# Kernel optimization log

Hardware: AMD Instinct MI355X
Metric: run time of the kernel (lower is better)

The kernel has to match this reference:

```python
import jax, jax.numpy as jnp
import numpy as np

HIDDEN = 1024
HEADS = 16
HEAD_DIM = HIDDEN // HEADS
SCALE = HEAD_DIM ** -0.5
NEG_INF = -1e9  # finite stand-in for -inf so silu(masked) -> ~0 instead of NaN


def setup_inputs() -> dict:
    key = jax.random.key(0)
    ks = jax.random.split(key, 12)
    B, Sq, Sk = 2, 2048, 2048
    inp = {
        "query": jax.random.normal(ks[0], (B, Sq, HIDDEN), jnp.float32),
        "key": jax.random.normal(ks[1], (B, Sk, HIDDEN), jnp.float32),
        "value": jax.random.normal(ks[2], (B, Sk, HIDDEN), jnp.float32),
        "mask": jax.random.randint(ks[3], (B, 1, Sq, Sk), 0, 2, jnp.int32),
        # torch nn.Linear weights are [out_features, in_features]
        "Wq": jax.random.normal(ks[4], (HIDDEN, HIDDEN), jnp.float32) * 0.02,
        "bq": jax.random.normal(ks[5], (HIDDEN,), jnp.float32) * 0.02,
        "Wk": jax.random.normal(ks[6], (HIDDEN, HIDDEN), jnp.float32) * 0.02,
        "bk": jax.random.normal(ks[7], (HIDDEN,), jnp.float32) * 0.02,
        "Wv": jax.random.normal(ks[8], (HIDDEN, HIDDEN), jnp.float32) * 0.02,
        "bv": jax.random.normal(ks[9], (HIDDEN,), jnp.float32) * 0.02,
        "Wo": jax.random.normal(ks[10], (HIDDEN, HIDDEN), jnp.float32) * 0.02,
    }
    return inp


def _split_heads(x):
    B, S, _ = x.shape
    return x.reshape(B, S, HEADS, HEAD_DIM).transpose(0, 2, 1, 3)  # [B,H,S,D]


def reference(query, key, value, mask, Wq, bq, Wk, bk, Wv, bv, Wo):
    B, Sq, _ = query.shape
    q = _split_heads(query @ Wq.T + bq)   # [B,H,Sq,D]
    k = _split_heads(key @ Wk.T + bk)     # [B,H,Sk,D]
    v = _split_heads(value @ Wv.T + bv)   # [B,H,Sk,D]
    scores = jnp.einsum("bhqd,bhkd->bhqk", q, k) * SCALE
    scores = jnp.where(mask == 0, NEG_INF, scores)
    attn = jax.nn.silu(scores)            # silu in place of softmax (per source)
    # dropout is identity in eval mode
    out = jnp.einsum("bhqk,bhkd->bhqd", attn, v)
    out = out.transpose(0, 2, 1, 3).reshape(B, Sq, HIDDEN)
    return out @ Wo.T  # o_proj has no bias
```

## Files before the change

kernel.cpp:

```cpp
#include <hip/hip_runtime.h>
#include <hip/hip_bf16.h>

typedef __attribute__((ext_vector_type(4))) float f32x4;
typedef __attribute__((ext_vector_type(16))) float f32x16;
typedef __attribute__((ext_vector_type(8))) short short8;
typedef __attribute__((ext_vector_type(4))) unsigned int uint4v;

__device__ __forceinline__ unsigned short f2bf(float f) {
  unsigned int u = __float_as_uint(f);
  u += 0x7fffu + ((u >> 16) & 1u);
  return (unsigned short)(u >> 16);
}

__device__ __forceinline__ void g2lds16(const void* g, void* l) {
  __builtin_amdgcn_global_load_lds(
      (const __attribute__((address_space(1))) void*)g,
      (__attribute__((address_space(3))) void*)l, 16, 0, 0);
}

__global__ __launch_bounds__(256) void cvt3(const float* __restrict__ s0,
                                            const float* __restrict__ s1,
                                            const float* __restrict__ s2,
                                            unsigned short* __restrict__ d0,
                                            unsigned short* __restrict__ d1,
                                            unsigned short* __restrict__ d2) {
  const int i = blockIdx.x * 256 + threadIdx.x;
  const float* s = blockIdx.y == 0 ? s0 : (blockIdx.y == 1 ? s1 : s2);
  unsigned short* d = blockIdx.y == 0 ? d0 : (blockIdx.y == 1 ? d1 : d2);
  const float4 v = ((const float4*)s)[i];
  ushort4 o;
  o.x = f2bf(v.x); o.y = f2bf(v.y); o.z = f2bf(v.z); o.w = f2bf(v.w);
  ((ushort4*)d)[i] = o;
}

__global__ __launch_bounds__(256) void cvt4(const float* __restrict__ s0,
                                            const float* __restrict__ s1,
                                            const float* __restrict__ s2,
                                            const float* __restrict__ s3,
                                            unsigned short* __restrict__ d0,
                                            unsigned short* __restrict__ d1,
                                            unsigned short* __restrict__ d2,
                                            unsigned short* __restrict__ d3) {
  const int i = blockIdx.x * 256 + threadIdx.x;
  const float* s = blockIdx.y == 0 ? s0 : (blockIdx.y == 1 ? s1 : (blockIdx.y == 2 ? s2 : s3));
  unsigned short* d = blockIdx.y == 0 ? d0 : (blockIdx.y == 1 ? d1 : (blockIdx.y == 2 ? d2 : d3));
  const float4 v = ((const float4*)s)[i];
  ushort4 o;
  o.x = f2bf(v.x); o.y = f2bf(v.y); o.z = f2bf(v.z); o.w = f2bf(v.w);
  ((ushort4*)d)[i] = o;
}

__global__ __launch_bounds__(256) void pack_mask(const int* __restrict__ mask,
                                                 unsigned long long* __restrict__ mb) {
  int i = blockIdx.x * 256 + threadIdx.x;
  unsigned long long bits = __ballot(mask[i] != 0);
  if ((threadIdx.x & 63) == 0) mb[i >> 6] = bits;
}

__global__ __launch_bounds__(256) void add_bf16(const unsigned short* __restrict__ a,
                                                const unsigned short* __restrict__ b,
                                                unsigned short* __restrict__ o) {
  const int i = blockIdx.x * 256 + threadIdx.x;
  const short8 va = ((const short8*)a)[i];
  const short8 vb = ((const short8*)b)[i];
  short8 vo;
#pragma unroll
  for (int j = 0; j < 8; ++j) {
    const float fa = __uint_as_float((unsigned int)(unsigned short)va[j] << 16);
    const float fb = __uint_as_float((unsigned int)(unsigned short)vb[j] << 16);
    vo[j] = (short)f2bf(fa + fb);
  }
  ((short8*)o)[i] = vo;
}

template <int BIAS_MODE, int OUT_BF16>
__device__ __forceinline__ void gemm_tile(
    unsigned short* __restrict__ As, unsigned short* __restrict__ Bs,
    const unsigned short* __restrict__ A, const unsigned short* __restrict__ B,
    const float* __restrict__ bias, void* __restrict__ Cp,
    const int N, const int K, const int m0, const int n0, const float cscale) {
  const int tid  = (int)threadIdx.x;
  const int lane = tid & 63;
  const int wm   = tid >> 7;
  const int wn   = (tid >> 6) & 1;

  const f32x4 vzero = {0.f, 0.f, 0.f, 0.f};
  f32x4 acc[4][4];
#pragma unroll
  for (int mr = 0; mr < 4; ++mr)
#pragma unroll
    for (int nr = 0; nr < 4; ++nr) acc[mr][nr] = vzero;

  for (int k0 = 0; k0 < K; k0 += 64) {
#pragma unroll
    for (int i = 0; i < 4; ++i) {
      const int idx = i * 256 + tid;
      const int r = idx >> 3;
      const int c = idx & 7;
      const int koff = k0 + ((c ^ (r & 7)) << 3);
      g2lds16(A + (size_t)(m0 + r) * K + koff, &As[(i * 256 + (tid & 192)) * 8]);
      g2lds16(B + (size_t)(n0 + r) * K + koff, &Bs[(i * 256 + (tid & 192)) * 8]);
    }
    __syncthreads();
#pragma unroll
    for (int kk = 0; kk < 2; ++kk) {
      short8 af[4], bf[4];
#pragma unroll
      for (int mr = 0; mr < 4; ++mr) {
        const int row = wm * 64 + mr * 16 + (lane & 15);
        const int ch = (kk * 4 + (lane >> 4)) ^ (row & 7);
        af[mr] = *(const short8*)&As[row * 64 + ch * 8];
      }
#pragma unroll
      for (int nr = 0; nr < 4; ++nr) {
        const int row = wn * 64 + nr * 16 + (lane & 15);
        const int ch = (kk * 4 + (lane >> 4)) ^ (row & 7);
        bf[nr] = *(const short8*)&Bs[row * 64 + ch * 8];
      }
#pragma unroll
      for (int mr = 0; mr < 4; ++mr)
#pragma unroll
        for (int nr = 0; nr < 4; ++nr)
          acc[mr][nr] = __builtin_amdgcn_mfma_f32_16x16x32_bf16(af[mr], bf[nr],
                                                                acc[mr][nr], 0, 0, 0);
    }
    __syncthreads();
  }

#pragma unroll
  for (int mr = 0; mr < 4; ++mr) {
#pragma unroll
    for (int nr = 0; nr < 4; ++nr) {
#pragma unroll
      for (int rg = 0; rg < 4; ++rg) {
        const int row = m0 + wm * 64 + mr * 16 + ((lane >> 4) << 2) + rg;
        const int col = n0 + wn * 64 + nr * 16 + (lane & 15);
        float v = acc[mr][nr][rg];
        if (BIAS_MODE == 1) v += bias[col];
        if (BIAS_MODE == 2) v += bias[row];
        v *= cscale;
        if (OUT_BF16) ((unsigned short*)Cp)[(size_t)row * N + col] = f2bf(v);
        else          ((float*)Cp)[(size_t)row * N + col] = v;
      }
    }
  }
}

#define QSCALE 0.18033688011112042f
#define LN2    0.6931471805599453f

__global__ __launch_bounds__(256) void proj_qkv(
    const unsigned short* __restrict__ xq, const unsigned short* __restrict__ xk,
    const unsigned short* __restrict__ xv,
    const unsigned short* __restrict__ wq, const unsigned short* __restrict__ wk,
    const unsigned short* __restrict__ wv,
    const float* __restrict__ bq, const float* __restrict__ bk,
    const float* __restrict__ bv,
    unsigned short* __restrict__ qp, unsigned short* __restrict__ kp,
    unsigned short* __restrict__ vt) {
  __shared__ unsigned short As[128 * 64];
  __shared__ unsigned short Bs[128 * 64];
  const int z = blockIdx.z;
  if (z == 0) {
    gemm_tile<1, 1>(As, Bs, xq, wq, bq, qp, 1024, 1024, blockIdx.y * 128, blockIdx.x * 128, QSCALE);
  } else if (z == 1) {
    gemm_tile<1, 1>(As, Bs, xk, wk, bk, kp, 1024, 1024, blockIdx.y * 128, blockIdx.x * 128, 1.0f);
  } else {
    gemm_tile<2, 1>(As, Bs, wv, xv, bv, vt, 4096, 1024, blockIdx.x * 128, blockIdx.y * 128, 1.0f);
  }
}

__global__ __launch_bounds__(256) void out_proj(
    const unsigned short* __restrict__ ao, const unsigned short* __restrict__ wo,
    float* __restrict__ out) {
  __shared__ unsigned short As[128 * 64];
  __shared__ unsigned short Bs[128 * 64];
  gemm_tile<0, 0>(As, Bs, ao, wo, nullptr, out, 1024, 1024, blockIdx.y * 128, blockIdx.x * 128, 1.0f);
}

__global__ __launch_bounds__(256, 4) void attn_kernel(
    const unsigned short* __restrict__ qp, const unsigned short* __restrict__ kp,
    const unsigned short* __restrict__ vt, const unsigned long long* __restrict__ mb,
    unsigned short* __restrict__ ao0, unsigned short* __restrict__ ao1) {
  __shared__ unsigned short Ks[2][64 * 64];
  __shared__ unsigned short Vts[2][64 * 64];

  const int tid  = (int)threadIdx.x;
  const int lane = tid & 63;
  const int w    = tid >> 6;
  const int c32  = lane & 31;
  const int lo   = lane >> 5;
  const int qbase = blockIdx.x * 128;
  const int h  = blockIdx.y;
  const int b  = blockIdx.z >> 1;
  const int ks = blockIdx.z & 1;
  const size_t tok0 = (size_t)b * 2048;
  const int kbase = ks * 1024;

  const int q = qbase + w * 32 + c32;
  const unsigned short* qptr = qp + (tok0 + q) * 1024 + h * 64 + lo * 8;
  short8 qf[4];
#pragma unroll
  for (int kd = 0; kd < 4; ++kd) qf[kd] = *(const short8*)(qptr + kd * 16);

  const unsigned long long* mql = mb + (tok0 + q) * 32 + ks * 16;

  f32x16 oacc[2];
#pragma unroll
  for (int dt = 0; dt < 2; ++dt)
#pragma unroll
    for (int r = 0; r < 16; ++r) oacc[dt][r] = 0.f;

  auto stage = [&](int kt_, int bf_) {
#pragma unroll
    for (int i = 0; i < 2; ++i) {
      const int idx = i * 256 + tid;
      const int r = idx >> 3;
      const int cc = idx & 7;
      const int cs = (cc ^ (r & 7)) << 3;
      g2lds16(kp + (tok0 + kbase + kt_ * 64 + r) * 1024 + h * 64 + cs,
              &Ks[bf_][(i * 256 + (tid & 192)) * 8]);
      g2lds16(vt + (size_t)(h * 64 + r) * 4096 + tok0 + kbase + kt_ * 64 + cs,
              &Vts[bf_][(i * 256 + (tid & 192)) * 8]);
    }
  };

  stage(0, 0);
  unsigned long long mcur = mql[0];
  __syncthreads();

  const f32x16 z16 = {0.f};
  int buf = 0;
  for (int kt = 0; kt < 16; ++kt) {
    if (kt < 15) stage(kt + 1, buf ^ 1);
    const unsigned long long mnext = (kt < 15) ? mql[kt + 1] : 0ULL;

    f32x16 st[2];
    st[0] = z16; st[1] = z16;
    __builtin_amdgcn_s_setprio(1);
#pragma unroll
    for (int kd = 0; kd < 4; ++kd) {
      const int ch = ((2 * kd + lo) ^ (c32 & 7)) << 3;
      const short8 kf0 = *(const short8*)&Ks[buf][c32 * 64 + ch];
      const short8 kf1 = *(const short8*)&Ks[buf][(32 + c32) * 64 + ch];
      st[0] = __builtin_amdgcn_mfma_f32_32x32x16_bf16(kf0, qf[kd], st[0], 0, 0, 0);
      st[1] = __builtin_amdgcn_mfma_f32_32x32x16_bf16(kf1, qf[kd], st[1], 0, 0, 0);
    }
    __builtin_amdgcn_s_setprio(0);

#pragma unroll
    for (int t = 0; t < 2; ++t) {
      const unsigned int ms = (unsigned int)(mcur >> (t * 32 + lo * 4));
#pragma unroll
      for (int r = 0; r < 16; ++r) {
        const int krow = (r & 3) + 8 * (r >> 2);
        const int smear = __builtin_amdgcn_sbfe((int)ms, krow, 1);
        const float sv = __int_as_float(__float_as_int(st[t][r]) & smear);
        st[t][r] = sv * __builtin_amdgcn_rcpf(1.f + __builtin_amdgcn_exp2f(-sv));
      }

      unsigned int u[8];
#pragma unroll
      for (int g = 0; g < 4; ++g) {
        asm("v_cvt_pk_bf16_f32 %0, %1, %2" : "=v"(u[2 * g])     : "v"(st[t][4 * g]),     "v"(st[t][4 * g + 1]));
        asm("v_cvt_pk_bf16_f32 %0, %1, %2" : "=v"(u[2 * g + 1]) : "v"(st[t][4 * g + 2]), "v"(st[t][4 * g + 3]));
      }
      asm("v_permlane32_swap_b32 %0, %1" : "+v"(u[0]), "+v"(u[2]));
      asm("v_permlane32_swap_b32 %0, %1" : "+v"(u[1]), "+v"(u[3]));
      asm("v_permlane32_swap_b32 %0, %1" : "+v"(u[4]), "+v"(u[6]));
      asm("v_permlane32_swap_b32 %0, %1" : "+v"(u[5]), "+v"(u[7]));
      const uint4v wA = {u[0], u[1], u[2], u[3]};
      const uint4v wB = {u[4], u[5], u[6], u[7]};
      const short8 paA = __builtin_bit_cast(short8, wA);
      const short8 paB = __builtin_bit_cast(short8, wB);

      __builtin_amdgcn_s_setprio(1);
#pragma unroll
      for (int dt = 0; dt < 2; ++dt) {
        const int drow = dt * 32 + c32;
        const short8 vf0 = *(const short8*)&Vts[buf][drow * 64 + (((4 * t + lo) ^ (c32 & 7)) << 3)];
        const short8 vf1 = *(const short8*)&Vts[buf][drow * 64 + (((4 * t + 2 + lo) ^ (c32 & 7)) << 3)];
        oacc[dt] = __builtin_amdgcn_mfma_f32_32x32x16_bf16(paA, vf0, oacc[dt], 0, 0, 0);
        oacc[dt] = __builtin_amdgcn_mfma_f32_32x32x16_bf16(paB, vf1, oacc[dt], 0, 0, 0);
      }
      __builtin_amdgcn_s_setprio(0);
    }

    mcur = mnext;
    __syncthreads();
    buf ^= 1;
  }

  unsigned short* aop = ks ? ao1 : ao0;
#pragma unroll
  for (int dt = 0; dt < 2; ++dt) {
#pragma unroll
    for (int r = 0; r < 16; ++r) {
      const int row = qbase + w * 32 + (r & 3) + 8 * (r >> 2) + 4 * lo;
      const int col = h * 64 + dt * 32 + c32;
      aop[(tok0 + row) * 1024 + col] = f2bf(oacc[dt][r] * LN2);
    }
  }
}

extern "C" void kernel_launch(void* const* d_in, const int* in_sizes, int n_in,
                              void* d_out, int out_size, void* d_ws, size_t ws_size,
                              hipStream_t stream) {
  (void)in_sizes; (void)n_in; (void)out_size; (void)ws_size;
  const float* query = (const float*)d_in[0];
  const float* key   = (const float*)d_in[1];
  const float* value = (const float*)d_in[2];
  const int*   mask  = (const int*)d_in[3];
  const float* Wq = (const float*)d_in[4];
  const float* bq = (const float*)d_in[5];
  const float* Wk = (const float*)d_in[6];
  const float* bk = (const float*)d_in[7];
  const float* Wv = (const float*)d_in[8];
  const float* bv = (const float*)d_in[9];
  const float* Wo = (const float*)d_in[10];

  char* ws = (char*)d_ws;
  const size_t MB = 1024 * 1024;
  unsigned short* xq  = (unsigned short*)(ws + 0 * MB);
  unsigned short* xk  = (unsigned short*)(ws + 8 * MB);
  unsigned short* xv  = (unsigned short*)(ws + 16 * MB);
  unsigned short* wqb = (unsigned short*)(ws + 24 * MB);
  unsigned short* wkb = (unsigned short*)(ws + 26 * MB);
  unsigned short* wvb = (unsigned short*)(ws + 28 * MB);
  unsigned short* wob = (unsigned short*)(ws + 30 * MB);
  unsigned short* qp  = (unsigned short*)(ws + 32 * MB);
  unsigned short* kp  = (unsigned short*)(ws + 40 * MB);
  unsigned short* vt  = (unsigned short*)(ws + 48 * MB);
  unsigned long long* mbq = (unsigned long long*)(ws + 56 * MB);
  unsigned short* ao  = xq;
  unsigned short* ap0 = xk;
  unsigned short* ap1 = xv;

  cvt3<<<dim3(4096, 3), 256, 0, stream>>>(query, key, value, xq, xk, xv);
  cvt4<<<dim3(1024, 4), 256, 0, stream>>>(Wq, Wk, Wv, Wo, wqb, wkb, wvb, wob);
  pack_mask<<<32768, 256, 0, stream>>>(mask, mbq);

  proj_qkv<<<dim3(8, 32, 3), 256, 0, stream>>>(xq, xk, xv, wqb, wkb, wvb,
                                               bq, bk, bv, qp, kp, vt);
  attn_kernel<<<dim3(16, 16, 4), 256, 0, stream>>>(qp, kp, vt, mbq, ap0, ap1);
  add_bf16<<<2048, 256, 0, stream>>>(ap0, ap1, ao);
  out_proj<<<dim3(8, 32), 256, 0, stream>>>(ao, wob, (float*)d_out);
}
```

Before: 171.5 us.

## Split key dimension across extra waves in attention and out-projection, fuse prep kernels

```diff
diff --git a/kernel.cpp b/kernel.cpp
--- a/kernel.cpp
+++ b/kernel.cpp
@@ -18,43 +18,42 @@
       (__attribute__((address_space(3))) void*)l, 16, 0, 0);
 }
 
-__global__ __launch_bounds__(256) void cvt3(const float* __restrict__ s0,
-                                            const float* __restrict__ s1,
-                                            const float* __restrict__ s2,
-                                            unsigned short* __restrict__ d0,
-                                            unsigned short* __restrict__ d1,
-                                            unsigned short* __restrict__ d2) {
-  const int i = blockIdx.x * 256 + threadIdx.x;
-  const float* s = blockIdx.y == 0 ? s0 : (blockIdx.y == 1 ? s1 : s2);
-  unsigned short* d = blockIdx.y == 0 ? d0 : (blockIdx.y == 1 ? d1 : d2);
-  const float4 v = ((const float4*)s)[i];
+__global__ __launch_bounds__(256) void prep(
+    const float* __restrict__ q, const float* __restrict__ k,
+    const float* __restrict__ v, const float* __restrict__ Wq,
+    const float* __restrict__ Wk, const float* __restrict__ Wv,
+    const float* __restrict__ Wo, const int* __restrict__ mask,
+    unsigned short* __restrict__ xq, unsigned short* __restrict__ xk,
+    unsigned short* __restrict__ xv, unsigned short* __restrict__ wqb,
+    unsigned short* __restrict__ wkb, unsigned short* __restrict__ wvb,
+    unsigned short* __restrict__ wob, unsigned long long* __restrict__ mb) {
+  const int y = blockIdx.y;
+  const int idx = blockIdx.x * 256 + (int)threadIdx.x;
+  if (y == 4) {
+#pragma unroll
+    for (int it = 0; it < 8; ++it) {
+      const int i = blockIdx.x * 2048 + it * 256 + (int)threadIdx.x;
+      const unsigned long long bits = __ballot(mask[i] != 0);
+      if ((threadIdx.x & 63) == 0) mb[i >> 6] = bits;
+    }
+    return;
+  }
+  const float* s;
+  unsigned short* d;
+  int i = idx;
+  if (y == 0)      { s = q; d = xq; }
+  else if (y == 1) { s = k; d = xk; }
+  else if (y == 2) { s = v; d = xv; }
+  else {
+    const int wsel = idx >> 18;
+    i = idx & 0x3FFFF;
+    s = wsel == 0 ? Wq : (wsel == 1 ? Wk : (wsel == 2 ? Wv : Wo));
+    d = wsel == 0 ? wqb : (wsel == 1 ? wkb : (wsel == 2 ? wvb : wob));
+  }
+  const float4 val = ((const float4*)s)[i];
   ushort4 o;
-  o.x = f2bf(v.x); o.y = f2bf(v.y); o.z = f2bf(v.z); o.w = f2bf(v.w);
+  o.x = f2bf(val.x); o.y = f2bf(val.y); o.z = f2bf(val.z); o.w = f2bf(val.w);
   ((ushort4*)d)[i] = o;
-}
-
-__global__ __launch_bounds__(256) void cvt4(const float* __restrict__ s0,
-                                            const float* __restrict__ s1,
-                                            const float* __restrict__ s2,
-                                            const float* __restrict__ s3,
-                                            unsigned short* __restrict__ d0,
-                                            unsigned short* __restrict__ d1,
-                                            unsigned short* __restrict__ d2,
-                                            unsigned short* __restrict__ d3) {
-  const int i = blockIdx.x * 256 + threadIdx.x;
-  const float* s = blockIdx.y == 0 ? s0 : (blockIdx.y == 1 ? s1 : (blockIdx.y == 2 ? s2 : s3));
-  unsigned short* d = blockIdx.y == 0 ? d0 : (blockIdx.y == 1 ? d1 : (blockIdx.y == 2 ? d2 : d3));
-  const float4 v = ((const float4*)s)[i];
-  ushort4 o;
-  o.x = f2bf(v.x); o.y = f2bf(v.y); o.z = f2bf(v.z); o.w = f2bf(v.w);
-  ((ushort4*)d)[i] = o;
-}
-
-__global__ __launch_bounds__(256) void pack_mask(const int* __restrict__ mask,
-                                                 unsigned long long* __restrict__ mb) {
-  int i = blockIdx.x * 256 + threadIdx.x;
-  unsigned long long bits = __ballot(mask[i] != 0);
-  if ((threadIdx.x & 63) == 0) mb[i >> 6] = bits;
 }
 
 __global__ __launch_bounds__(256) void add_bf16(const unsigned short* __restrict__ a,
@@ -170,24 +169,104 @@
   }
 }
 
-__global__ __launch_bounds__(256) void out_proj(
+__global__ __launch_bounds__(512) void out_proj8(
     const unsigned short* __restrict__ ao, const unsigned short* __restrict__ wo,
     float* __restrict__ out) {
-  __shared__ unsigned short As[128 * 64];
-  __shared__ unsigned short Bs[128 * 64];
-  gemm_tile<0, 0>(As, Bs, ao, wo, nullptr, out, 1024, 1024, blockIdx.y * 128, blockIdx.x * 128, 1.0f);
-}
-
-__global__ __launch_bounds__(256, 4) void attn_kernel(
+  __shared__ unsigned short SM[4][128 * 64];
+
+  const int tid  = (int)threadIdx.x;
+  const int lane = tid & 63;
+  const int wm = tid >> 8;
+  const int wn = (tid >> 7) & 1;
+  const int kh = (tid >> 6) & 1;
+  const int m0 = blockIdx.y * 128;
+  const int n0 = blockIdx.x * 128;
+
+  const f32x4 vzero = {0.f, 0.f, 0.f, 0.f};
+  f32x4 acc[4][4];
+#pragma unroll
+  for (int mr = 0; mr < 4; ++mr)
+#pragma unroll
+    for (int nr = 0; nr < 4; ++nr) acc[mr][nr] = vzero;
+
+  for (int j = 0; j < 8; ++j) {
+#pragma unroll
+    for (int i = 0; i < 2; ++i) {
+      const int idx = i * 512 + tid;
+      const int r = idx >> 3;
+      const int cc = idx & 7;
+      const int cs = (cc ^ (r & 7)) << 3;
+      const int wb = (i * 512 + (tid & 448)) * 8;
+      g2lds16(ao + (size_t)(m0 + r) * 1024 + j * 64 + cs,       &SM[0][wb]);
+      g2lds16(ao + (size_t)(m0 + r) * 1024 + 512 + j * 64 + cs, &SM[1][wb]);
+      g2lds16(wo + (size_t)(n0 + r) * 1024 + j * 64 + cs,       &SM[2][wb]);
+      g2lds16(wo + (size_t)(n0 + r) * 1024 + 512 + j * 64 + cs, &SM[3][wb]);
+    }
+    __syncthreads();
+#pragma unroll
+    for (int kk = 0; kk < 2; ++kk) {
+      short8 af[4], bf[4];
+#pragma unroll
+      for (int mr = 0; mr < 4; ++mr) {
+        const int row = wm * 64 + mr * 16 + (lane & 15);
+        const int ch = (kk * 4 + (lane >> 4)) ^ (row & 7);
+        af[mr] = *(const short8*)&SM[kh][row * 64 + ch * 8];
+      }
+#pragma unroll
+      for (int nr = 0; nr < 4; ++nr) {
+        const int row = wn * 64 + nr * 16 + (lane & 15);
+        const int ch = (kk * 4 + (lane >> 4)) ^ (row & 7);
+        bf[nr] = *(const short8*)&SM[2 + kh][row * 64 + ch * 8];
+      }
+#pragma unroll
+      for (int mr = 0; mr < 4; ++mr)
+#pragma unroll
+        for (int nr = 0; nr < 4; ++nr)
+          acc[mr][nr] = __builtin_amdgcn_mfma_f32_16x16x32_bf16(af[mr], bf[nr],
+                                                                acc[mr][nr], 0, 0, 0);
+    }
+    __syncthreads();
+  }
+
+  float* red = (float*)SM;
+  const int reg4 = wm * 2 + wn;
+  if (kh) {
+#pragma unroll
+    for (int mr = 0; mr < 4; ++mr)
+#pragma unroll
+      for (int nr = 0; nr < 4; ++nr)
+#pragma unroll
+        for (int g = 0; g < 4; ++g)
+          red[reg4 * 4096 + lane * 64 + ((mr * 16 + nr * 4 + g + lane) & 63)] = acc[mr][nr][g];
+  }
+  __syncthreads();
+  if (!kh) {
+#pragma unroll
+    for (int mr = 0; mr < 4; ++mr)
+#pragma unroll
+      for (int nr = 0; nr < 4; ++nr)
+#pragma unroll
+        for (int g = 0; g < 4; ++g) {
+          const float v = acc[mr][nr][g] +
+              red[reg4 * 4096 + lane * 64 + ((mr * 16 + nr * 4 + g + lane) & 63)];
+          const int row = m0 + wm * 64 + mr * 16 + ((lane >> 4) << 2) + g;
+          const int col = n0 + wn * 64 + nr * 16 + (lane & 15);
+          out[(size_t)row * 1024 + col] = v;
+        }
+  }
+}
+
+__global__ __launch_bounds__(512, 4) void attn_kernel(
     const unsigned short* __restrict__ qp, const unsigned short* __restrict__ kp,
     const unsigned short* __restrict__ vt, const unsigned long long* __restrict__ mb,
     unsigned short* __restrict__ ao0, unsigned short* __restrict__ ao1) {
-  __shared__ unsigned short Ks[2][64 * 64];
-  __shared__ unsigned short Vts[2][64 * 64];
+  __shared__ unsigned short SMEM[2][2][64 * 64];
 
   const int tid  = (int)threadIdx.x;
   const int lane = tid & 63;
   const int w    = tid >> 6;
+  const int qsub = w >> 1;
+  const int kh   = w & 1;
   const int c32  = lane & 31;
   const int lo   = lane >> 5;
   const int qbase = blockIdx.x * 128;
@@ -197,7 +276,7 @@
   const size_t tok0 = (size_t)b * 2048;
   const int kbase = ks * 1024;
 
-  const int q = qbase + w * 32 + c32;
+  const int q = qbase + qsub * 32 + c32;
   const unsigned short* qptr = qp + (tok0 + q) * 1024 + h * 64 + lo * 8;
   short8 qf[4];
 #pragma unroll
@@ -212,17 +291,12 @@
     for (int r = 0; r < 16; ++r) oacc[dt][r] = 0.f;
 
   auto stage = [&](int kt_, int bf_) {
-#pragma unroll
-    for (int i = 0; i < 2; ++i) {
-      const int idx = i * 256 + tid;
-      const int r = idx >> 3;
-      const int cc = idx & 7;
-      const int cs = (cc ^ (r & 7)) << 3;
-      g2lds16(kp + (tok0 + kbase + kt_ * 64 + r) * 1024 + h * 64 + cs,
-              &Ks[bf_][(i * 256 + (tid & 192)) * 8]);
-      g2lds16(vt + (size_t)(h * 64 + r) * 4096 + tok0 + kbase + kt_ * 64 + cs,
-              &Vts[bf_][(i * 256 + (tid & 192)) * 8]);
-    }
+    const int r = tid >> 3;
+    const int cc = tid & 7;
+    const int cs = (cc ^ (r & 7)) << 3;
+    const int wb = (tid & 448) * 8;
+    g2lds16(kp + (tok0 + kbase + kt_ * 64 + r) * 1024 + h * 64 + cs, &SMEM[bf_][0][wb]);
+    g2lds16(vt + (size_t)(h * 64 + r) * 4096 + tok0 + kbase + kt_ * 64 + cs, &SMEM[bf_][1][wb]);
   };
 
   stage(0, 0);
@@ -235,71 +309,77 @@
     if (kt < 15) stage(kt + 1, buf ^ 1);
     const unsigned long long mnext = (kt < 15) ? mql[kt + 1] : 0ULL;
 
-    f32x16 st[2];
-    st[0] = z16; st[1] = z16;
+    f32x16 st = z16;
     __builtin_amdgcn_s_setprio(1);
 #pragma unroll
     for (int kd = 0; kd < 4; ++kd) {
-      const int ch = ((2 * kd + lo) ^ (c32 & 7)) << 3;
-      const short8 kf0 = *(const short8*)&Ks[buf][c32 * 64 + ch];
-      const short8 kf1 = *(const short8*)&Ks[buf][(32 + c32) * 64 + ch];
-      st[0] = __builtin_amdgcn_mfma_f32_32x32x16_bf16(kf0, qf[kd], st[0], 0, 0, 0);
-      st[1] = __builtin_amdgcn_mfma_f32_32x32x16_bf16(kf1, qf[kd], st[1], 0, 0, 0);
+      const int krt = kh * 32 + c32;
+      const short8 kf = *(const short8*)&SMEM[buf][0][krt * 64 + (((2 * kd + lo) ^ (c32 & 7)) << 3)];
+      st = __builtin_amdgcn_mfma_f32_32x32x16_bf16(kf, qf[kd], st, 0, 0, 0);
     }
     __builtin_amdgcn_s_setprio(0);
 
-#pragma unroll
-    for (int t = 0; t < 2; ++t) {
-      const unsigned int ms = (unsigned int)(mcur >> (t * 32 + lo * 4));
-#pragma unroll
-      for (int r = 0; r < 16; ++r) {
-        const int krow = (r & 3) + 8 * (r >> 2);
-        const int smear = __builtin_amdgcn_sbfe((int)ms, krow, 1);
-        const float sv = __int_as_float(__float_as_int(st[t][r]) & smear);
-        st[t][r] = sv * __builtin_amdgcn_rcpf(1.f + __builtin_amdgcn_exp2f(-sv));
-      }
-
-      unsigned int u[8];
-#pragma unroll
-      for (int g = 0; g < 4; ++g) {
-        asm("v_cvt_pk_bf16_f32 %0, %1, %2" : "=v"(u[2 * g])     : "v"(st[t][4 * g]),     "v"(st[t][4 * g + 1]));
-        asm("v_cvt_pk_bf16_f32 %0, %1, %2" : "=v"(u[2 * g + 1]) : "v"(st[t][4 * g + 2]), "v"(st[t][4 * g + 3]));
-      }
-      asm("v_permlane32_swap_b32 %0, %1" : "+v"(u[0]), "+v"(u[2]));
-      asm("v_permlane32_swap_b32 %0, %1" : "+v"(u[1]), "+v"(u[3]));
-      asm("v_permlane32_swap_b32 %0, %1" : "+v"(u[4]), "+v"(u[6]));
-      asm("v_permlane32_swap_b32 %0, %1" : "+v"(u[5]), "+v"(u[7]));
-      const uint4v wA = {u[0], u[1], u[2], u[3]};
-      const uint4v wB = {u[4], u[5], u[6], u[7]};
-      const short8 paA = __builtin_bit_cast(short8, wA);
-      const short8 paB = __builtin_bit_cast(short8, wB);
-
-      __builtin_amdgcn_s_setprio(1);
-#pragma unroll
-      for (int dt = 0; dt < 2; ++dt) {
-        const int drow = dt * 32 + c32;
-        const short8 vf0 = *(const short8*)&Vts[buf][drow * 64 + (((4 * t + lo) ^ (c32 & 7)) << 3)];
-        const short8 vf1 = *(const short8*)&Vts[buf][drow * 64 + (((4 * t + 2 + lo) ^ (c32 & 7)) << 3)];
-        oacc[dt] = __builtin_amdgcn_mfma_f32_32x32x16_bf16(paA, vf0, oacc[dt], 0, 0, 0);
-        oacc[dt] = __builtin_amdgcn_mfma_f32_32x32x16_bf16(paB, vf1, oacc[dt], 0, 0, 0);
-      }
-      __builtin_amdgcn_s_setprio(0);
-    }
+    const unsigned int ms = (unsigned int)(mcur >> (kh * 32 + lo * 4));
+#pragma unroll
+    for (int r = 0; r < 16; ++r) {
+      const int krow = (r & 3) + 8 * (r >> 2);
+      const int smear = __builtin_amdgcn_sbfe((int)ms, krow, 1);
+      const float sv = __int_as_float(__float_as_int(st[r]) & smear);
+      st[r] = sv * __builtin_amdgcn_rcpf(1.f + __builtin_amdgcn_exp2f(-sv));
+    }
+
+    unsigned int u[8];
+#pragma unroll
+    for (int g = 0; g < 4; ++g) {
+      asm("v_cvt_pk_bf16_f32 %0, %1, %2" : "=v"(u[2 * g])     : "v"(st[4 * g]),     "v"(st[4 * g + 1]));
+      asm("v_cvt_pk_bf16_f32 %0, %1, %2" : "=v"(u[2 * g + 1]) : "v"(st[4 * g + 2]), "v"(st[4 * g + 3]));
+    }
+    asm("v_permlane32_swap_b32 %0, %1" : "+v"(u[0]), "+v"(u[2]));
+    asm("v_permlane32_swap_b32 %0, %1" : "+v"(u[1]), "+v"(u[3]));
+    asm("v_permlane32_swap_b32 %0, %1" : "+v"(u[4]), "+v"(u[6]));
+    asm("v_permlane32_swap_b32 %0, %1" : "+v"(u[5]), "+v"(u[7]));
+    const uint4v wA = {u[0], u[1], u[2], u[3]};
+    const uint4v wB = {u[4], u[5], u[6], u[7]};
+    const short8 paA = __builtin_bit_cast(short8, wA);
+    const short8 paB = __builtin_bit_cast(short8, wB);
+
+    __builtin_amdgcn_s_setprio(1);
+#pragma unroll
+    for (int dt = 0; dt < 2; ++dt) {
+      const int drow = dt * 32 + c32;
+      const short8 vf0 = *(const short8*)&SMEM[buf][1][drow * 64 + (((4 * kh + lo) ^ (c32 & 7)) << 3)];
+      const short8 vf1 = *(const short8*)&SMEM[buf][1][drow * 64 + (((4 * kh + 2 + lo) ^ (c32 & 7)) << 3)];
+      oacc[dt] = __builtin_amdgcn_mfma_f32_32x32x16_bf16(paA, vf0, oacc[dt], 0, 0, 0);
+      oacc[dt] = __builtin_amdgcn_mfma_f32_32x32x16_bf16(paB, vf1, oacc[dt], 0, 0, 0);
+    }
+    __builtin_amdgcn_s_setprio(0);
 
     mcur = mnext;
     __syncthreads();
     buf ^= 1;
   }
 
-  unsigned short* aop = ks ? ao1 : ao0;
-#pragma unroll
-  for (int dt = 0; dt < 2; ++dt) {
-#pragma unroll
-    for (int r = 0; r < 16; ++r) {
-      const int row = qbase + w * 32 + (r & 3) + 8 * (r >> 2) + 4 * lo;
-      const int col = h * 64 + dt * 32 + c32;
-      aop[(tok0 + row) * 1024 + col] = f2bf(oacc[dt][r] * LN2);
-    }
+  float* red = (float*)SMEM;
+  const int rbase = qsub * 2048;
+  if (kh) {
+#pragma unroll
+    for (int dt = 0; dt < 2; ++dt)
+#pragma unroll
+      for (int r = 0; r < 16; ++r)
+        red[rbase + lane * 32 + ((dt * 16 + r + lane) & 31)] = oacc[dt][r];
+  }
+  __syncthreads();
+  if (!kh) {
+    unsigned short* aop = ks ? ao1 : ao0;
+#pragma unroll
+    for (int dt = 0; dt < 2; ++dt)
+#pragma unroll
+      for (int r = 0; r < 16; ++r) {
+        const float o2 = oacc[dt][r] + red[rbase + lane * 32 + ((dt * 16 + r + lane) & 31)];
+        const int row = qbase + qsub * 32 + (r & 3) + 8 * (r >> 2) + 4 * lo;
+        const int col = h * 64 + dt * 32 + c32;
+        aop[(tok0 + row) * 1024 + col] = f2bf(o2 * LN2);
+      }
   }
 }
 
@@ -336,13 +416,12 @@
   unsigned short* ap0 = xk;
   unsigned short* ap1 = xv;
 
-  cvt3<<<dim3(4096, 3), 256, 0, stream>>>(query, key, value, xq, xk, xv);
-  cvt4<<<dim3(1024, 4), 256, 0, stream>>>(Wq, Wk, Wv, Wo, wqb, wkb, wvb, wob);
-  pack_mask<<<32768, 256, 0, stream>>>(mask, mbq);
+  prep<<<dim3(4096, 5), 256, 0, stream>>>(query, key, value, Wq, Wk, Wv, Wo, mask,
+                                          xq, xk, xv, wqb, wkb, wvb, wob, mbq);
 
   proj_qkv<<<dim3(8, 32, 3), 256, 0, stream>>>(xq, xk, xv, wqb, wkb, wvb,
                                                bq, bk, bv, qp, kp, vt);
-  attn_kernel<<<dim3(16, 16, 4), 256, 0, stream>>>(qp, kp, vt, mbq, ap0, ap1);
+  attn_kernel<<<dim3(16, 16, 4), 512, 0, stream>>>(qp, kp, vt, mbq, ap0, ap1);
   add_bf16<<<2048, 256, 0, stream>>>(ap0, ap1, ao);
-  out_proj<<<dim3(8, 32), 256, 0, stream>>>(ao, wob, (float*)d_out);
-}
+  out_proj8<<<dim3(8, 32), 512, 0, stream>>>(ao, wob, (float*)d_out);
+}
```

New measurement: 160.4 us. -6.4%, faster.
